# Optimization experiments

Measured on AMD Instinct MI355X. Metric: run time of the kernel, lower is better.

The kernel has to match this reference:

```python
import jax, jax.numpy as jnp
import numpy as np

B, T, D, E, H = 4, 2048, 1024, 8, 1024

def setup_inputs() -> dict:
    key = jax.random.key(0)
    k1, k2, k3, k4, k5 = jax.random.split(key, 5)
    s = 1.0 / np.sqrt(D)
    return {
        "x": jax.random.normal(k1, (B, T, D), dtype=jnp.float32),
        "Wg": jax.random.normal(k2, (E, D), dtype=jnp.float32) * s,
        "gate_bank": jax.random.normal(k3, (E, D, H), dtype=jnp.float32) * s,
        "up_bank": jax.random.normal(k4, (E, D, H), dtype=jnp.float32) * s,
        "down_bank": jax.random.normal(k5, (E, H, D), dtype=jnp.float32) * (1.0 / np.sqrt(H)),
    }

def reference(x, Wg, gate_bank, up_bank, down_bank):
    # gate logits: [B,T,E]  (nn.Linear with weight [E,D], no bias; eval mode -> no noise)
    logits = jnp.einsum('btd,ed->bte', x, Wg)
    selected = jnp.argmax(logits, axis=-1)            # [B,T] top-1 expert id
    # dense all-expert SwiGLU (faithful to the original math)
    a = jnp.einsum('btd,edh->bteh', x, gate_bank)     # [B,T,E,H]
    u = jnp.einsum('btd,edh->bteh', x, up_bank)       # [B,T,E,H]
    h = jax.nn.silu(a) * u                            # [B,T,E,H]
    y_all = jnp.einsum('bteh,ehd->bted', h, down_bank)  # [B,T,E,D]
    # top-1 gather of the selected expert's output
    idx = selected[:, :, None, None]                  # [B,T,1,1]
    y = jnp.take_along_axis(y_all, idx, axis=2)[:, :, 0, :]  # [B,T,D]
    return y
```

## Files before the change

### kernel.cpp

```cpp
#include <hip/hip_runtime.h>
#include <hip/hip_bf16.h>

typedef __attribute__((ext_vector_type(8))) short bf16x8;
typedef __attribute__((ext_vector_type(4))) float f32x4;
typedef __attribute__((ext_vector_type(4))) short sh4;

static constexpr int NTOK = 8192;
static constexpr int D = 1024;
static constexpr int E = 8;
static constexpr int H = 1024;
static constexpr int BM = 128, BN = 128, BK = 32;
static constexpr int BN1 = 64;
static constexpr int NWAVE = NTOK / 64;
static constexpr int MSLOT = 16;

__device__ __forceinline__ unsigned short f2bf(float f) {
  unsigned u = __builtin_bit_cast(unsigned, f);
  u = (u + 0x7FFFu + ((u >> 16) & 1u)) >> 16;
  return (unsigned short)u;
}

__device__ __forceinline__ void gload16(const void* g, void* l) {
  __builtin_amdgcn_global_load_lds(
      (const __attribute__((address_space(1))) unsigned int*)g,
      (__attribute__((address_space(3))) unsigned int*)l, 16, 0, 0);
}

__device__ __forceinline__ void expert_span(const int* __restrict__ counts,
                                            int e, int& off, int& cnt) {
  off = 0; cnt = 0;
#pragma unroll
  for (int i = 0; i < E; ++i) {
    int ci = counts[i];
    off += (i < e) ? ci : 0;
    cnt = (i == e) ? ci : cnt;
  }
}

__global__ __launch_bounds__(256) void k_router_cvt(
    const float* __restrict__ x, const float* __restrict__ Wg,
    unsigned short* __restrict__ xb, int* __restrict__ sel) {
  __shared__ float wgs[E * D];
  int tid = threadIdx.x;
  const float4* wg4 = (const float4*)Wg;
  float4* ws4 = (float4*)wgs;
  for (int i = tid; i < E * D / 4; i += 256) ws4[i] = wg4[i];
  __syncthreads();
  int lane = tid & 63;
  int t = blockIdx.x * 4 + (tid >> 6);
  const float4* xr = (const float4*)(x + (size_t)t * D);
  unsigned short* xo = xb + (size_t)t * D;
  float acc[E];
#pragma unroll
  for (int e = 0; e < E; ++e) acc[e] = 0.f;
#pragma unroll
  for (int j = 0; j < 4; ++j) {
    int idx = j * 64 + lane;
    float4 v = xr[idx];
    sh4 o;
    o.x = (short)f2bf(v.x); o.y = (short)f2bf(v.y);
    o.z = (short)f2bf(v.z); o.w = (short)f2bf(v.w);
    *(sh4*)(xo + idx * 4) = o;
#pragma unroll
    for (int e = 0; e < E; ++e) {
      float4 wv = *(const float4*)&wgs[e * D + idx * 4];
      acc[e] += v.x * wv.x + v.y * wv.y + v.z * wv.z + v.w * wv.w;
    }
  }
#pragma unroll
  for (int e = 0; e < E; ++e) {
#pragma unroll
    for (int off = 32; off; off >>= 1) acc[e] += __shfl_xor(acc[e], off, 64);
  }
  if (lane == 0) {
    int best = 0; float bv = acc[0];
#pragma unroll
    for (int e = 1; e < E; ++e) if (acc[e] > bv) { bv = acc[e]; best = e; }
    sel[t] = best;
  }
}

__global__ __launch_bounds__(256) void k_wavecnt(
    const int* __restrict__ sel, int* __restrict__ wcnt) {
  int t = blockIdx.x * 256 + threadIdx.x;
  int lane = threadIdx.x & 63;
  int gwave = t >> 6;
  int s = sel[t];
#pragma unroll
  for (int e = 0; e < E; ++e) {
    unsigned long long m = __ballot(s == e);
    if (lane == 0) wcnt[e * NWAVE + gwave] = __popcll(m);
  }
}

__global__ __launch_bounds__(128) void k_scan(
    const int* __restrict__ wcnt, int* __restrict__ wbase,
    int* __restrict__ counts) {
  __shared__ int cnt[E][NWAVE];
  __shared__ int pre[E][NWAVE];
  __shared__ int eoff[E + 1];
  int tid = threadIdx.x;
#pragma unroll
  for (int e = 0; e < E; ++e) cnt[e][tid] = wcnt[e * NWAVE + tid];
  __syncthreads();
  if (tid < E) {
    int s = 0;
    for (int w = 0; w < NWAVE; ++w) { pre[tid][w] = s; s += cnt[tid][w]; }
    counts[tid] = s;
  }
  __syncthreads();
  if (tid == 0) {
    int s = 0;
#pragma unroll
    for (int e = 0; e < E; ++e) { eoff[e] = s; s += counts[e]; }
    eoff[E] = s;
  }
  __syncthreads();
#pragma unroll
  for (int e = 0; e < E; ++e) wbase[e * NWAVE + tid] = eoff[e] + pre[e][tid];
}

__global__ __launch_bounds__(256) void k_scatter(
    const int* __restrict__ sel, const int* __restrict__ wbase,
    int* __restrict__ tlist) {
  int t = blockIdx.x * 256 + threadIdx.x;
  int lane = threadIdx.x & 63;
  int gwave = t >> 6;
  int s = sel[t];
  unsigned long long below = (lane == 63) ? 0x7FFFFFFFFFFFFFFFull
                                          : ((1ull << lane) - 1ull);
  int rank = 0, base = 0;
#pragma unroll
  for (int e = 0; e < E; ++e) {
    unsigned long long m = __ballot(s == e);
    int r = __popcll(m & below);
    int b = wbase[e * NWAVE + gwave];
    rank = (e == s) ? r : rank;
    base = (e == s) ? b : base;
  }
  tlist[base + rank] = t;
}

__global__ __launch_bounds__(256) void k_transpose_banks(
    const float* __restrict__ gate, const float* __restrict__ up,
    const float* __restrict__ down, unsigned short* __restrict__ gt,
    unsigned short* __restrict__ ut, unsigned short* __restrict__ dt) {
  int m = blockIdx.z;
  int mm = m & 7;
  const size_t MS = (size_t)1024 * 1024;
  const float* src;
  unsigned short* dst;
  if (m < 8)       { src = gate + mm * MS; dst = gt + mm * MS; }
  else if (m < 16) { src = up   + mm * MS; dst = ut + mm * MS; }
  else             { src = down + mm * MS; dst = dt + mm * MS; }
  __shared__ unsigned short T[64][72];
  int tid = threadIdx.x;
  int r = tid >> 2;
  int cs = (tid & 3) * 16;
  int tk0 = blockIdx.x * 64, tn0 = blockIdx.y * 64;
  const float* s0 = src + (size_t)(tk0 + r) * 1024 + tn0 + cs;
#pragma unroll
  for (int q = 0; q < 4; ++q) {
    float4 v = *(const float4*)(s0 + q * 4);
    sh4 o;
    o.x = (short)f2bf(v.x); o.y = (short)f2bf(v.y);
    o.z = (short)f2bf(v.z); o.w = (short)f2bf(v.w);
    *(sh4*)&T[r][cs + q * 4] = o;
  }
  __syncthreads();
  unsigned short* d0 = dst + (size_t)(tn0 + r) * 1024 + tk0 + cs;
#pragma unroll
  for (int q = 0; q < 4; ++q) {
    sh4 w;
    w.x = (short)T[cs + q * 4 + 0][r];
    w.y = (short)T[cs + q * 4 + 1][r];
    w.z = (short)T[cs + q * 4 + 2][r];
    w.w = (short)T[cs + q * 4 + 3][r];
    *(sh4*)(d0 + q * 4) = w;
  }
}

__global__ __launch_bounds__(256, 3) void k_ffn1(
    const unsigned short* __restrict__ xb, const unsigned short* __restrict__ gt,
    const unsigned short* __restrict__ ut, const int* __restrict__ tlist,
    const int* __restrict__ counts, unsigned short* __restrict__ hbuf) {
  int e = blockIdx.x;
  int mt = blockIdx.y >> 4;
  int n0 = (blockIdx.y & 15) * BN1;
  int off, cnt;
  expert_span(counts, e, off, cnt);
  int rem = cnt - mt * BM;
  if (rem <= 0) return;
  if (rem > BM) rem = BM;
  int tid = threadIdx.x;
  int lane = tid & 63;
  int wid = tid >> 6;
  int wm = wid >> 1, wn = wid & 1;

  __shared__ unsigned short lds[3][8192];

  const unsigned short* gtb = gt + (size_t)e * D * H;
  const unsigned short* utb = ut + (size_t)e * D * H;

  int rr = lane >> 2;
  int skel = 8 * ((lane & 3) ^ (rr & 3) ^ ((rr >> 2) & 3));
  const unsigned short *gP, *uP, *tP[2];
  gP = gtb + (size_t)(n0 + wid * 16 + rr) * D + skel;
  uP = utb + (size_t)(n0 + wid * 16 + rr) * D + skel;
#pragma unroll
  for (int p = 0; p < 2; ++p) {
    int row = wid * 32 + p * 16 + rr;
    int tr = mt * BM + row; if (tr >= cnt) tr = cnt - 1;
    int tok = tlist[off + tr];
    tP[p] = xb + (size_t)tok * D + skel;
  }

  auto STAGE = [&](int buf, int k0) {
    unsigned short* b = &lds[buf][0];
    gload16(gP + k0, b + wid * 512);
    gload16(uP + k0, b + 2048 + wid * 512);
    gload16(tP[0] + k0, b + 4096 + wid * 1024);
    gload16(tP[1] + k0, b + 4096 + wid * 1024 + 512);
  };

  f32x4 accg[2][4], accu[2][4];
#pragma unroll
  for (int i = 0; i < 2; ++i)
#pragma unroll
    for (int j = 0; j < 4; ++j) { accg[i][j] = (f32x4)(0.f); accu[i][j] = (f32x4)(0.f); }

  int fr = lane & 15, s = lane >> 4;
  int swr = 8 * ((s ^ (fr & 3) ^ ((fr >> 2) & 3)) & 3);
  int woff = (wm * 32 + fr) * 32 + swr;
  int toff = 4096 + (wn * 64 + fr) * 32 + swr;

  constexpr int NS = D / BK;
  STAGE(0, 0);
  STAGE(1, BK);
  asm volatile("s_waitcnt vmcnt(4)" ::: "memory");
  __builtin_amdgcn_s_barrier();

  int bc = 0, bn_ = 2;
  for (int t = 0; t < NS; ++t) {
    int tn = t + 2; if (tn >= NS) tn = NS - 1;
    STAGE(bn_, tn * BK);
    const unsigned short* L = lds[bc];
    bf16x8 wg[2], wu[2], tf[4];
#pragma unroll
    for (int i = 0; i < 2; ++i) {
      wg[i] = *(const bf16x8*)(L + woff + i * 512);
      wu[i] = *(const bf16x8*)(L + 2048 + woff + i * 512);
    }
#pragma unroll
    for (int j = 0; j < 4; ++j) tf[j] = *(const bf16x8*)(L + toff + j * 512);
#pragma unroll
    for (int i = 0; i < 2; ++i)
#pragma unroll
      for (int j = 0; j < 4; ++j) {
        accg[i][j] = __builtin_amdgcn_mfma_f32_16x16x32_bf16(wg[i], tf[j], accg[i][j], 0, 0, 0);
        accu[i][j] = __builtin_amdgcn_mfma_f32_16x16x32_bf16(wu[i], tf[j], accu[i][j], 0, 0, 0);
      }
    asm volatile("s_waitcnt vmcnt(4)" ::: "memory");
    __builtin_amdgcn_s_barrier();
    bc = (bc == 2) ? 0 : bc + 1;
    bn_ = (bn_ == 2) ? 0 : bn_ + 1;
  }
  asm volatile("s_waitcnt vmcnt(0)" ::: "memory");

  int gr_base = off + mt * BM;
#pragma unroll
  for (int j = 0; j < 4; ++j) {
    int tl = wn * 64 + j * 16 + fr;
    if (tl < rem) {
      size_t tb = (size_t)(gr_base + tl) * H + n0 + wm * 32 + s * 4;
#pragma unroll
      for (int i = 0; i < 2; ++i) {
        sh4 v;
#pragma unroll
        for (int q = 0; q < 4; ++q) {
          float a = accg[i][j][q];
          float u = accu[i][j][q];
          float hv = (a / (1.f + __expf(-a))) * u;
          ((short*)&v)[q] = (short)f2bf(hv);
        }
        *(sh4*)(hbuf + tb + i * 16) = v;
      }
    }
  }
}

__global__ __launch_bounds__(256, 3) void k_ffn2(
    const unsigned short* __restrict__ hbuf, const unsigned short* __restrict__ dt,
    const int* __restrict__ tlist, const int* __restrict__ counts,
    float* __restrict__ y) {
  int e = blockIdx.x;
  int mt = blockIdx.y >> 3;
  int n0 = (blockIdx.y & 7) * BN;
  int off, cnt;
  expert_span(counts, e, off, cnt);
  int rem = cnt - mt * BM;
  if (rem <= 0) return;
  if (rem > BM) rem = BM;
  int tid = threadIdx.x;
  int lane = tid & 63;
  int wid = tid >> 6;
  int wm = wid >> 1, wn = wid & 1;

  __shared__ unsigned short lds[3][8192];

  const unsigned short* dtb = dt + (size_t)e * D * H;
  int gr0 = off + mt * BM;

  int rr = lane >> 2;
  int skel = 8 * ((lane & 3) ^ (rr & 3) ^ ((rr >> 2) & 3));
  const unsigned short *dP[2], *hP[2];
#pragma unroll
  for (int p = 0; p < 2; ++p) {
    int ch = wid * 2 + p;
    int row = ch * 16 + rr;
    dP[p] = dtb + (size_t)(n0 + row) * H + skel;
    hP[p] = hbuf + (size_t)(gr0 + row) * H + skel;
  }

  auto STAGE = [&](int buf, int k0) {
#pragma unroll
    for (int p = 0; p < 2; ++p) {
      int ch = wid * 2 + p;
      unsigned short* base = &lds[buf][ch * 512];
      gload16(dP[p] + k0, base);
      gload16(hP[p] + k0, base + 4096);
    }
  };

  f32x4 acc[4][4];
#pragma unroll
  for (int i = 0; i < 4; ++i)
#pragma unroll
    for (int j = 0; j < 4; ++j) acc[i][j] = (f32x4)(0.f);

  int fr = lane & 15, s = lane >> 4;
  int swr = 8 * ((s ^ (fr & 3) ^ ((fr >> 2) & 3)) & 3);
  int woff = (wm * 64 + fr) * 32 + swr;
  int toff = (wn * 64 + fr) * 32 + swr;

  constexpr int NS = H / BK;
  STAGE(0, 0);
  STAGE(1, BK);
  asm volatile("s_waitcnt vmcnt(4)" ::: "memory");
  __builtin_amdgcn_s_barrier();

  int bc = 0, bn_ = 2;
  for (int t = 0; t < NS; ++t) {
    int tn = t + 2; if (tn >= NS) tn = NS - 1;
    STAGE(bn_, tn * BK);
    const unsigned short* L = lds[bc];
    bf16x8 wd[4], tf[4];
#pragma unroll
    for (int i = 0; i < 4; ++i) {
      wd[i] = *(const bf16x8*)(L + woff + i * 512);
      tf[i] = *(const bf16x8*)(L + 4096 + toff + i * 512);
    }
#pragma unroll
    for (int i = 0; i < 4; ++i)
#pragma unroll
      for (int j = 0; j < 4; ++j)
        acc[i][j] = __builtin_amdgcn_mfma_f32_16x16x32_bf16(wd[i], tf[j], acc[i][j], 0, 0, 0);
    asm volatile("s_waitcnt vmcnt(4)" ::: "memory");
    __builtin_amdgcn_s_barrier();
    bc = (bc == 2) ? 0 : bc + 1;
    bn_ = (bn_ == 2) ? 0 : bn_ + 1;
  }
  asm volatile("s_waitcnt vmcnt(0)" ::: "memory");

#pragma unroll
  for (int j = 0; j < 4; ++j) {
    int tl = wn * 64 + j * 16 + fr;
    if (tl < rem) {
      int tok = tlist[off + mt * BM + tl];
      size_t tb = (size_t)tok * D + n0 + wm * 64 + s * 4;
#pragma unroll
      for (int i = 0; i < 4; ++i) {
        float4 v;
        v.x = acc[i][j][0]; v.y = acc[i][j][1];
        v.z = acc[i][j][2]; v.w = acc[i][j][3];
        *(float4*)(y + tb + i * 16) = v;
      }
    }
  }
}

extern "C" void kernel_launch(void* const* d_in, const int* in_sizes, int n_in,
                              void* d_out, int out_size, void* d_ws, size_t ws_size,
                              hipStream_t stream) {
  const float* x = (const float*)d_in[0];
  const float* Wg = (const float*)d_in[1];
  const float* gate = (const float*)d_in[2];
  const float* up = (const float*)d_in[3];
  const float* down = (const float*)d_in[4];
  float* y = (float*)d_out;

  char* ws = (char*)d_ws;
  int* counts = (int*)ws;
  int* sel = (int*)(ws + 1024);
  int* wcnt = (int*)(ws + 40960);
  int* wbase = (int*)(ws + 45056);
  int* tlist = (int*)(ws + 49152);
  size_t o = 131072;
  unsigned short* xb = (unsigned short*)(ws + o);  o += (size_t)NTOK * D * 2;
  unsigned short* gt = (unsigned short*)(ws + o);  o += (size_t)E * D * H * 2;
  unsigned short* ut = (unsigned short*)(ws + o);  o += (size_t)E * D * H * 2;
  unsigned short* dt = (unsigned short*)(ws + o);  o += (size_t)E * D * H * 2;
  unsigned short* hbuf = (unsigned short*)(ws + o);

  k_router_cvt<<<NTOK / 4, 256, 0, stream>>>(x, Wg, xb, sel);
  dim3 gt_grid(16, 16, 24);
  k_transpose_banks<<<gt_grid, 256, 0, stream>>>(gate, up, down, gt, ut, dt);
  k_wavecnt<<<NTOK / 256, 256, 0, stream>>>(sel, wcnt);
  k_scan<<<1, 128, 0, stream>>>(wcnt, wbase, counts);
  k_scatter<<<NTOK / 256, 256, 0, stream>>>(sel, wbase, tlist);
  dim3 g1(E, MSLOT * 16);
  k_ffn1<<<g1, 256, 0, stream>>>(xb, gt, ut, tlist, counts, hbuf);
  dim3 g2(E, MSLOT * 8);
  k_ffn2<<<g2, 256, 0, stream>>>(hbuf, dt, tlist, counts, y);
}
```

Measured before the change: 129.7 us.

## Merge router and bank-transpose kernels; switch FFN GEMMs to BK=64 double buffering

```diff
diff --git a/kernel.cpp b/kernel.cpp
--- a/kernel.cpp
+++ b/kernel.cpp
@@ -9,8 +9,8 @@
 static constexpr int D = 1024;
 static constexpr int E = 8;
 static constexpr int H = 1024;
-static constexpr int BM = 128, BN = 128, BK = 32;
-static constexpr int BN1 = 64;
+static constexpr int BM = 128;
+static constexpr int BK = 64;
 static constexpr int NWAVE = NTOK / 64;
 static constexpr int MSLOT = 16;
 
@@ -37,46 +37,87 @@
   }
 }
 
-__global__ __launch_bounds__(256) void k_router_cvt(
+__global__ __launch_bounds__(256) void k_prep(
     const float* __restrict__ x, const float* __restrict__ Wg,
-    unsigned short* __restrict__ xb, int* __restrict__ sel) {
-  __shared__ float wgs[E * D];
+    const float* __restrict__ gate, const float* __restrict__ up,
+    const float* __restrict__ down, unsigned short* __restrict__ xb,
+    int* __restrict__ sel, unsigned short* __restrict__ gt,
+    unsigned short* __restrict__ ut, unsigned short* __restrict__ dt) {
+  __shared__ char smem[32768];
+  int bid = blockIdx.x;
   int tid = threadIdx.x;
-  const float4* wg4 = (const float4*)Wg;
-  float4* ws4 = (float4*)wgs;
-  for (int i = tid; i < E * D / 4; i += 256) ws4[i] = wg4[i];
-  __syncthreads();
-  int lane = tid & 63;
-  int t = blockIdx.x * 4 + (tid >> 6);
-  const float4* xr = (const float4*)(x + (size_t)t * D);
-  unsigned short* xo = xb + (size_t)t * D;
-  float acc[E];
-#pragma unroll
-  for (int e = 0; e < E; ++e) acc[e] = 0.f;
-#pragma unroll
-  for (int j = 0; j < 4; ++j) {
-    int idx = j * 64 + lane;
-    float4 v = xr[idx];
-    sh4 o;
-    o.x = (short)f2bf(v.x); o.y = (short)f2bf(v.y);
-    o.z = (short)f2bf(v.z); o.w = (short)f2bf(v.w);
-    *(sh4*)(xo + idx * 4) = o;
+  if (bid < 6144) {
+    unsigned short (*T)[72] = (unsigned short(*)[72])smem;
+    int m = bid >> 8;
+    int rem2 = bid & 255;
+    int mm = m & 7;
+    const size_t MS = (size_t)1024 * 1024;
+    const float* src;
+    unsigned short* dst;
+    if (m < 8)       { src = gate + mm * MS; dst = gt + mm * MS; }
+    else if (m < 16) { src = up   + mm * MS; dst = ut + mm * MS; }
+    else             { src = down + mm * MS; dst = dt + mm * MS; }
+    int r = tid >> 2;
+    int cs = (tid & 3) * 16;
+    int tk0 = (rem2 & 15) * 64, tn0 = (rem2 >> 4) * 64;
+    const float* s0 = src + (size_t)(tk0 + r) * 1024 + tn0 + cs;
+#pragma unroll
+    for (int q = 0; q < 4; ++q) {
+      float4 v = *(const float4*)(s0 + q * 4);
+      sh4 o;
+      o.x = (short)f2bf(v.x); o.y = (short)f2bf(v.y);
+      o.z = (short)f2bf(v.z); o.w = (short)f2bf(v.w);
+      *(sh4*)&T[r][cs + q * 4] = o;
+    }
+    __syncthreads();
+    unsigned short* d0 = dst + (size_t)(tn0 + r) * 1024 + tk0 + cs;
+#pragma unroll
+    for (int q = 0; q < 4; ++q) {
+      sh4 w;
+      w.x = (short)T[cs + q * 4 + 0][r];
+      w.y = (short)T[cs + q * 4 + 1][r];
+      w.z = (short)T[cs + q * 4 + 2][r];
+      w.w = (short)T[cs + q * 4 + 3][r];
+      *(sh4*)(d0 + q * 4) = w;
+    }
+  } else {
+    float* wgs = (float*)smem;
+    const float4* wg4 = (const float4*)Wg;
+    float4* ws4 = (float4*)wgs;
+    for (int i = tid; i < E * D / 4; i += 256) ws4[i] = wg4[i];
+    __syncthreads();
+    int lane = tid & 63;
+    int t = (bid - 6144) * 4 + (tid >> 6);
+    const float4* xr = (const float4*)(x + (size_t)t * D);
+    unsigned short* xo = xb + (size_t)t * D;
+    float acc[E];
+#pragma unroll
+    for (int e = 0; e < E; ++e) acc[e] = 0.f;
+#pragma unroll
+    for (int j = 0; j < 4; ++j) {
+      int idx = j * 64 + lane;
+      float4 v = xr[idx];
+      sh4 o;
+      o.x = (short)f2bf(v.x); o.y = (short)f2bf(v.y);
+      o.z = (short)f2bf(v.z); o.w = (short)f2bf(v.w);
+      *(sh4*)(xo + idx * 4) = o;
+#pragma unroll
+      for (int e = 0; e < E; ++e) {
+        float4 wv = *(const float4*)&wgs[e * D + idx * 4];
+        acc[e] += v.x * wv.x + v.y * wv.y + v.z * wv.z + v.w * wv.w;
+      }
+    }
 #pragma unroll
     for (int e = 0; e < E; ++e) {
-      float4 wv = *(const float4*)&wgs[e * D + idx * 4];
-      acc[e] += v.x * wv.x + v.y * wv.y + v.z * wv.z + v.w * wv.w;
-    }
-  }
-#pragma unroll
-  for (int e = 0; e < E; ++e) {
-#pragma unroll
-    for (int off = 32; off; off >>= 1) acc[e] += __shfl_xor(acc[e], off, 64);
-  }
-  if (lane == 0) {
-    int best = 0; float bv = acc[0];
-#pragma unroll
-    for (int e = 1; e < E; ++e) if (acc[e] > bv) { bv = acc[e]; best = e; }
-    sel[t] = best;
+#pragma unroll
+      for (int off = 32; off; off >>= 1) acc[e] += __shfl_xor(acc[e], off, 64);
+    }
+    if (lane == 0) {
+      int best = 0; float bv = acc[0];
+#pragma unroll
+      for (int e = 1; e < E; ++e) if (acc[e] > bv) { bv = acc[e]; best = e; }
+      sel[t] = best;
+    }
   }
 }
 
@@ -141,52 +182,13 @@
   tlist[base + rank] = t;
 }
 
-__global__ __launch_bounds__(256) void k_transpose_banks(
-    const float* __restrict__ gate, const float* __restrict__ up,
-    const float* __restrict__ down, unsigned short* __restrict__ gt,
-    unsigned short* __restrict__ ut, unsigned short* __restrict__ dt) {
-  int m = blockIdx.z;
-  int mm = m & 7;
-  const size_t MS = (size_t)1024 * 1024;
-  const float* src;
-  unsigned short* dst;
-  if (m < 8)       { src = gate + mm * MS; dst = gt + mm * MS; }
-  else if (m < 16) { src = up   + mm * MS; dst = ut + mm * MS; }
-  else             { src = down + mm * MS; dst = dt + mm * MS; }
-  __shared__ unsigned short T[64][72];
-  int tid = threadIdx.x;
-  int r = tid >> 2;
-  int cs = (tid & 3) * 16;
-  int tk0 = blockIdx.x * 64, tn0 = blockIdx.y * 64;
-  const float* s0 = src + (size_t)(tk0 + r) * 1024 + tn0 + cs;
-#pragma unroll
-  for (int q = 0; q < 4; ++q) {
-    float4 v = *(const float4*)(s0 + q * 4);
-    sh4 o;
-    o.x = (short)f2bf(v.x); o.y = (short)f2bf(v.y);
-    o.z = (short)f2bf(v.z); o.w = (short)f2bf(v.w);
-    *(sh4*)&T[r][cs + q * 4] = o;
-  }
-  __syncthreads();
-  unsigned short* d0 = dst + (size_t)(tn0 + r) * 1024 + tk0 + cs;
-#pragma unroll
-  for (int q = 0; q < 4; ++q) {
-    sh4 w;
-    w.x = (short)T[cs + q * 4 + 0][r];
-    w.y = (short)T[cs + q * 4 + 1][r];
-    w.z = (short)T[cs + q * 4 + 2][r];
-    w.w = (short)T[cs + q * 4 + 3][r];
-    *(sh4*)(d0 + q * 4) = w;
-  }
-}
-
-__global__ __launch_bounds__(256, 3) void k_ffn1(
+__global__ __launch_bounds__(256, 2) void k_ffn1(
     const unsigned short* __restrict__ xb, const unsigned short* __restrict__ gt,
     const unsigned short* __restrict__ ut, const int* __restrict__ tlist,
     const int* __restrict__ counts, unsigned short* __restrict__ hbuf) {
   int e = blockIdx.x;
   int mt = blockIdx.y >> 4;
-  int n0 = (blockIdx.y & 15) * BN1;
+  int n0 = (blockIdx.y & 15) * 64;
   int off, cnt;
   expert_span(counts, e, off, cnt);
   int rem = cnt - mt * BM;
@@ -197,30 +199,39 @@
   int wid = tid >> 6;
   int wm = wid >> 1, wn = wid & 1;
 
-  __shared__ unsigned short lds[3][8192];
+  __shared__ unsigned short lds[2][16384];
 
   const unsigned short* gtb = gt + (size_t)e * D * H;
   const unsigned short* utb = ut + (size_t)e * D * H;
 
-  int rr = lane >> 2;
-  int skel = 8 * ((lane & 3) ^ (rr & 3) ^ ((rr >> 2) & 3));
-  const unsigned short *gP, *uP, *tP[2];
-  gP = gtb + (size_t)(n0 + wid * 16 + rr) * D + skel;
-  uP = utb + (size_t)(n0 + wid * 16 + rr) * D + skel;
-#pragma unroll
-  for (int p = 0; p < 2; ++p) {
-    int row = wid * 32 + p * 16 + rr;
+  int srow8 = lane >> 3;
+  int hs8 = ((lane & 7) ^ srow8) * 8;
+
+  const unsigned short *gS[2], *uS[2], *tS[4];
+#pragma unroll
+  for (int q = 0; q < 2; ++q) {
+    int row = wid * 16 + q * 8 + srow8;
+    gS[q] = gtb + (size_t)(n0 + row) * D + hs8;
+    uS[q] = utb + (size_t)(n0 + row) * D + hs8;
+  }
+#pragma unroll
+  for (int q = 0; q < 4; ++q) {
+    int row = wid * 32 + q * 8 + srow8;
     int tr = mt * BM + row; if (tr >= cnt) tr = cnt - 1;
     int tok = tlist[off + tr];
-    tP[p] = xb + (size_t)tok * D + skel;
+    tS[q] = xb + (size_t)tok * D + hs8;
   }
 
   auto STAGE = [&](int buf, int k0) {
     unsigned short* b = &lds[buf][0];
-    gload16(gP + k0, b + wid * 512);
-    gload16(uP + k0, b + 2048 + wid * 512);
-    gload16(tP[0] + k0, b + 4096 + wid * 1024);
-    gload16(tP[1] + k0, b + 4096 + wid * 1024 + 512);
+#pragma unroll
+    for (int q = 0; q < 2; ++q) {
+      gload16(gS[q] + k0, b + wid * 1024 + q * 512);
+      gload16(uS[q] + k0, b + 4096 + wid * 1024 + q * 512);
+    }
+#pragma unroll
+    for (int q = 0; q < 4; ++q)
+      gload16(tS[q] + k0, b + 8192 + wid * 2048 + q * 512);
   };
 
   f32x4 accg[2][4], accu[2][4];
@@ -230,40 +241,42 @@
     for (int j = 0; j < 4; ++j) { accg[i][j] = (f32x4)(0.f); accu[i][j] = (f32x4)(0.f); }
 
   int fr = lane & 15, s = lane >> 4;
-  int swr = 8 * ((s ^ (fr & 3) ^ ((fr >> 2) & 3)) & 3);
-  int woff = (wm * 32 + fr) * 32 + swr;
-  int toff = 4096 + (wn * 64 + fr) * 32 + swr;
+  int x8 = fr & 7;
+  int so0 = ((s ^ x8) & 7) * 8;
+  int so1 = (((4 + s) ^ x8) & 7) * 8;
 
   constexpr int NS = D / BK;
   STAGE(0, 0);
-  STAGE(1, BK);
-  asm volatile("s_waitcnt vmcnt(4)" ::: "memory");
-  __builtin_amdgcn_s_barrier();
-
-  int bc = 0, bn_ = 2;
   for (int t = 0; t < NS; ++t) {
-    int tn = t + 2; if (tn >= NS) tn = NS - 1;
-    STAGE(bn_, tn * BK);
-    const unsigned short* L = lds[bc];
-    bf16x8 wg[2], wu[2], tf[4];
-#pragma unroll
-    for (int i = 0; i < 2; ++i) {
-      wg[i] = *(const bf16x8*)(L + woff + i * 512);
-      wu[i] = *(const bf16x8*)(L + 2048 + woff + i * 512);
-    }
-#pragma unroll
-    for (int j = 0; j < 4; ++j) tf[j] = *(const bf16x8*)(L + toff + j * 512);
-#pragma unroll
-    for (int i = 0; i < 2; ++i)
+    int tn = t + 1; if (tn >= NS) tn = NS - 1;
+    STAGE((t + 1) & 1, tn * BK);
+    asm volatile("s_waitcnt vmcnt(8)" ::: "memory");
+    __builtin_amdgcn_s_barrier();
+    const unsigned short* L = lds[t & 1];
+#pragma unroll
+    for (int ks = 0; ks < 2; ++ks) {
+      int so = ks ? so1 : so0;
+      bf16x8 wg[2], wu[2], tf[4];
+#pragma unroll
+      for (int i = 0; i < 2; ++i) {
+        int R = wm * 32 + i * 16 + fr;
+        wg[i] = *(const bf16x8*)(L + R * 64 + so);
+        wu[i] = *(const bf16x8*)(L + 4096 + R * 64 + so);
+      }
 #pragma unroll
       for (int j = 0; j < 4; ++j) {
-        accg[i][j] = __builtin_amdgcn_mfma_f32_16x16x32_bf16(wg[i], tf[j], accg[i][j], 0, 0, 0);
-        accu[i][j] = __builtin_amdgcn_mfma_f32_16x16x32_bf16(wu[i], tf[j], accu[i][j], 0, 0, 0);
-      }
-    asm volatile("s_waitcnt vmcnt(4)" ::: "memory");
+        int R = wn * 64 + j * 16 + fr;
+        tf[j] = *(const bf16x8*)(L + 8192 + R * 64 + so);
+      }
+#pragma unroll
+      for (int i = 0; i < 2; ++i)
+#pragma unroll
+        for (int j = 0; j < 4; ++j) {
+          accg[i][j] = __builtin_amdgcn_mfma_f32_16x16x32_bf16(wg[i], tf[j], accg[i][j], 0, 0, 0);
+          accu[i][j] = __builtin_amdgcn_mfma_f32_16x16x32_bf16(wu[i], tf[j], accu[i][j], 0, 0, 0);
+        }
+    }
     __builtin_amdgcn_s_barrier();
-    bc = (bc == 2) ? 0 : bc + 1;
-    bn_ = (bn_ == 2) ? 0 : bn_ + 1;
   }
   asm volatile("s_waitcnt vmcnt(0)" ::: "memory");
 
@@ -289,13 +302,13 @@
   }
 }
 
-__global__ __launch_bounds__(256, 3) void k_ffn2(
+__global__ __launch_bounds__(256, 2) void k_ffn2(
     const unsigned short* __restrict__ hbuf, const unsigned short* __restrict__ dt,
     const int* __restrict__ tlist, const int* __restrict__ counts,
     float* __restrict__ y) {
   int e = blockIdx.x;
   int mt = blockIdx.y >> 3;
-  int n0 = (blockIdx.y & 7) * BN;
+  int n0 = (blockIdx.y & 7) * 128;
   int off, cnt;
   expert_span(counts, e, off, cnt);
   int rem = cnt - mt * BM;
@@ -306,29 +319,28 @@
   int wid = tid >> 6;
   int wm = wid >> 1, wn = wid & 1;
 
-  __shared__ unsigned short lds[3][8192];
+  __shared__ unsigned short lds[2][16384];
 
   const unsigned short* dtb = dt + (size_t)e * D * H;
   int gr0 = off + mt * BM;
 
-  int rr = lane >> 2;
-  int skel = 8 * ((lane & 3) ^ (rr & 3) ^ ((rr >> 2) & 3));
-  const unsigned short *dP[2], *hP[2];
-#pragma unroll
-  for (int p = 0; p < 2; ++p) {
-    int ch = wid * 2 + p;
-    int row = ch * 16 + rr;
-    dP[p] = dtb + (size_t)(n0 + row) * H + skel;
-    hP[p] = hbuf + (size_t)(gr0 + row) * H + skel;
+  int srow8 = lane >> 3;
+  int hs8 = ((lane & 7) ^ srow8) * 8;
+
+  const unsigned short *dS[4], *tS[4];
+#pragma unroll
+  for (int q = 0; q < 4; ++q) {
+    int row = wid * 32 + q * 8 + srow8;
+    dS[q] = dtb + (size_t)(n0 + row) * H + hs8;
+    tS[q] = hbuf + (size_t)(gr0 + row) * H + hs8;
   }
 
   auto STAGE = [&](int buf, int k0) {
-#pragma unroll
-    for (int p = 0; p < 2; ++p) {
-      int ch = wid * 2 + p;
-      unsigned short* base = &lds[buf][ch * 512];
-      gload16(dP[p] + k0, base);
-      gload16(hP[p] + k0, base + 4096);
+    unsigned short* b = &lds[buf][0];
+#pragma unroll
+    for (int q = 0; q < 4; ++q) {
+      gload16(dS[q] + k0, b + wid * 2048 + q * 512);
+      gload16(tS[q] + k0, b + 8192 + wid * 2048 + q * 512);
     }
   };
 
@@ -339,36 +351,39 @@
     for (int j = 0; j < 4; ++j) acc[i][j] = (f32x4)(0.f);
 
   int fr = lane & 15, s = lane >> 4;
-  int swr = 8 * ((s ^ (fr & 3) ^ ((fr >> 2) & 3)) & 3);
-  int woff = (wm * 64 + fr) * 32 + swr;
-  int toff = (wn * 64 + fr) * 32 + swr;
+  int x8 = fr & 7;
+  int so0 = ((s ^ x8) & 7) * 8;
+  int so1 = (((4 + s) ^ x8) & 7) * 8;
 
   constexpr int NS = H / BK;
   STAGE(0, 0);
-  STAGE(1, BK);
-  asm volatile("s_waitcnt vmcnt(4)" ::: "memory");
-  __builtin_amdgcn_s_barrier();
-
-  int bc = 0, bn_ = 2;
   for (int t = 0; t < NS; ++t) {
-    int tn = t + 2; if (tn >= NS) tn = NS - 1;
-    STAGE(bn_, tn * BK);
-    const unsigned short* L = lds[bc];
-    bf16x8 wd[4], tf[4];
-#pragma unroll
-    for (int i = 0; i < 4; ++i) {
-      wd[i] = *(const bf16x8*)(L + woff + i * 512);
-      tf[i] = *(const bf16x8*)(L + 4096 + toff + i * 512);
-    }
-#pragma unroll
-    for (int i = 0; i < 4; ++i)
-#pragma unroll
-      for (int j = 0; j < 4; ++j)
-        acc[i][j] = __builtin_amdgcn_mfma_f32_16x16x32_bf16(wd[i], tf[j], acc[i][j], 0, 0, 0);
-    asm volatile("s_waitcnt vmcnt(4)" ::: "memory");
+    int tn = t + 1; if (tn >= NS) tn = NS - 1;
+    STAGE((t + 1) & 1, tn * BK);
+    asm volatile("s_waitcnt vmcnt(8)" ::: "memory");
     __builtin_amdgcn_s_barrier();
-    bc = (bc == 2) ? 0 : bc + 1;
-    bn_ = (bn_ == 2) ? 0 : bn_ + 1;
+    const unsigned short* L = lds[t & 1];
+#pragma unroll
+    for (int ks = 0; ks < 2; ++ks) {
+      int so = ks ? so1 : so0;
+      bf16x8 wd[4], tf[4];
+#pragma unroll
+      for (int i = 0; i < 4; ++i) {
+        int R = wm * 64 + i * 16 + fr;
+        wd[i] = *(const bf16x8*)(L + R * 64 + so);
+      }
+#pragma unroll
+      for (int j = 0; j < 4; ++j) {
+        int R = wn * 64 + j * 16 + fr;
+        tf[j] = *(const bf16x8*)(L + 8192 + R * 64 + so);
+      }
+#pragma unroll
+      for (int i = 0; i < 4; ++i)
+#pragma unroll
+        for (int j = 0; j < 4; ++j)
+          acc[i][j] = __builtin_amdgcn_mfma_f32_16x16x32_bf16(wd[i], tf[j], acc[i][j], 0, 0, 0);
+    }
+    __builtin_amdgcn_s_barrier();
   }
   asm volatile("s_waitcnt vmcnt(0)" ::: "memory");
 
@@ -412,9 +427,7 @@
   unsigned short* dt = (unsigned short*)(ws + o);  o += (size_t)E * D * H * 2;
   unsigned short* hbuf = (unsigned short*)(ws + o);
 
-  k_router_cvt<<<NTOK / 4, 256, 0, stream>>>(x, Wg, xb, sel);
-  dim3 gt_grid(16, 16, 24);
-  k_transpose_banks<<<gt_grid, 256, 0, stream>>>(gate, up, down, gt, ut, dt);
+  k_prep<<<6144 + NTOK / 4, 256, 0, stream>>>(x, Wg, gate, up, down, xb, sel, gt, ut, dt);
   k_wavecnt<<<NTOK / 256, 256, 0, stream>>>(sel, wcnt);
   k_scan<<<1, 128, 0, stream>>>(wcnt, wbase, counts);
   k_scatter<<<NTOK / 256, 256, 0, stream>>>(sel, wbase, tlist);
```

New measurement: 116.9 us. 9.9% less time.
